# Optimization experiments

Measured on AMD Instinct MI355X. Metric: run time of the kernel, lower is better.

Reference implementation:

```python
import jax, jax.numpy as jnp
import numpy as np

# ---- config (matches init_kwargs) ----
C_IN, C_OUT = 128, 128
HYPER_OUT = 64            # hyper_out_size in DoubleConv
KB = C_IN // HYPER_OUT    # k = 2 blocks along input channels
HB = C_OUT // HYPER_OUT   # h = 2 blocks along output channels
Z_DIM, HID, SEIDEL_DIM = 128, 128, 48
R, F = 8, 3               # num_radii, filter size
BN_EPS = 1e-5


def _mlp_bank(z, W1, b1, W2, b2):
    # z: (S,); W1: (M,S,HID); returns (M, HID) embeddings from M distinct MLPs
    h = jax.nn.relu(jnp.einsum('s,msh->mh', z, W1) + b1)
    return jax.nn.relu(jnp.einsum('mh,mhg->mg', h, W2) + b2)


def _hyper(e, hw2, hb2, hw1, hb1):
    # Ha-style hypernetwork: e (Z_DIM,) -> kernel (64, 64, R, F, F)
    h_in = (e @ hw2 + hb2).reshape(HYPER_OUT, Z_DIM)
    h_fin = h_in @ hw1 + hb1  # (64, 64*R*F*F)
    return h_fin.reshape(HYPER_OUT, HYPER_OUT, R, F, F)


def _assemble(kernels, rows, cols):
    # kernels: (rows*cols, 64, 64, R, F, F) -> (rows*64, cols*64, R, F, F)
    k = kernels.reshape(rows, cols, HYPER_OUT, HYPER_OUT, R, F, F)
    k = k.transpose(0, 2, 1, 3, 4, 5, 6)
    return k.reshape(rows * HYPER_OUT, cols * HYPER_OUT, R, F, F)


def _interp_radii(w, Wdim):
    # trilinear interpolate (R,F,F)->(Wdim,F,F); F->F is identity, so linear along R
    # align_corners=False (PyTorch default)
    src = (jnp.arange(Wdim, dtype=jnp.float32) + 0.5) * (R / Wdim) - 0.5
    src = jnp.clip(src, 0.0, R - 1.0)
    i0 = jnp.floor(src).astype(jnp.int32)
    i1 = jnp.minimum(i0 + 1, R - 1)
    t = (src - i0.astype(jnp.float32))[None, None, :, None, None]
    return w[:, :, i0] * (1.0 - t) + w[:, :, i1] * t  # (co, ci, Wdim, F, F)


def _lri_conv(x, w):
    # x: (c_in, H, W); w: (c_out, c_in, R, F, F); padding=1, k=3
    c_in, H, W = x.shape
    xp = jnp.concatenate([x[:, -1:, :], x, x[:, :1, :]], axis=1)  # circular pad H
    xp = jnp.pad(xp, ((0, 0), (0, 0), (1, 1)))                    # zero pad W
    # patches laid out (c, di, dj) to match F.unfold
    pat = jnp.stack([xp[:, di:di + H, dj:dj + W]
                     for di in range(3) for dj in range(3)], axis=1)  # (c_in, 9, H, W)
    pat = pat.reshape(c_in * 9, H, W).transpose(1, 2, 0)              # (H, W, c_in*9)
    wi = _interp_radii(w, W)                                          # (co, ci, W, F, F)
    wu = wi.transpose(0, 2, 1, 3, 4).reshape(w.shape[0], W, c_in * 9) # (co, W, ci*9)
    return jnp.einsum('hwj,cwj->chw', pat, wu)                        # (co, H, W)


def _bn_eval(x, gamma, beta):
    # eval-mode BatchNorm2d with running_mean=0, running_var=1
    scale = gamma / jnp.sqrt(1.0 + BN_EPS)
    return x * scale[:, None, None] + beta[:, None, None]


def setup_inputs() -> dict:
    key = jax.random.key(0)
    ks = jax.random.split(key, 20)
    B, H, W = 2, 256, 128
    n1 = HB * KB   # 4 MLPs for first conv
    n2 = HB * HB   # 4 MLPs for second conv
    inp = {
        'x': jax.random.normal(ks[0], (B, C_IN, H, W), jnp.float32),
        'seidel': jax.random.normal(ks[1], (B, SEIDEL_DIM), jnp.float32),
        'm1_W1': jax.random.normal(ks[2], (n1, SEIDEL_DIM, HID)) * 0.1,
        'm1_b1': jnp.zeros((n1, HID)),
        'm1_W2': jax.random.normal(ks[3], (n1, HID, HID)) * 0.08,
        'm1_b2': jnp.zeros((n1, HID)),
        'm2_W1': jax.random.normal(ks[4], (n2, SEIDEL_DIM, HID)) * 0.1,
        'm2_b1': jnp.zeros((n2, HID)),
        'm2_W2': jax.random.normal(ks[5], (n2, HID, HID)) * 0.08,
        'm2_b2': jnp.zeros((n2, HID)),
        'hyp_w2': jax.random.normal(ks[6], (Z_DIM, HYPER_OUT * Z_DIM)) * 0.02,
        'hyp_b2': jnp.zeros((HYPER_OUT * Z_DIM,)),
        'hyp_w1': jax.random.normal(ks[7], (Z_DIM, HYPER_OUT * R * F * F)) * 0.02,
        'hyp_b1': jnp.zeros((HYPER_OUT * R * F * F,)),
        'bn1_g': jnp.ones((C_OUT,)), 'bn1_b': jnp.zeros((C_OUT,)),
        'bn2_g': jnp.ones((C_OUT,)), 'bn2_b': jnp.zeros((C_OUT,)),
    }
    return inp


def reference(x, seidel, m1_W1, m1_b1, m1_W2, m1_b2, m2_W1, m2_b1, m2_W2, m2_b2,
              hyp_w2, hyp_b2, hyp_w1, hyp_b1, bn1_g, bn1_b, bn2_g, bn2_b):
    hyper = lambda e: _hyper(e, hyp_w2, hyp_b2, hyp_w1, hyp_b1)

    def one_sample(x_i, z_i):
        emb1 = _mlp_bank(z_i, m1_W1, m1_b1, m1_W2, m1_b2)   # (h*k, Z)
        w1 = _assemble(jax.vmap(hyper)(emb1), HB, KB)        # (c_out, c_in, R, F, F)
        emb2 = _mlp_bank(z_i, m2_W1, m2_b1, m2_W2, m2_b2)   # (h*h, Z)
        w2 = _assemble(jax.vmap(hyper)(emb2), HB, HB)        # (c_out, c_out, R, F, F)
        y = jax.nn.relu(_bn_eval(_lri_conv(x_i, w1), bn1_g, bn1_b))
        y = jax.nn.relu(_bn_eval(_lri_conv(y, w2), bn2_g, bn2_b))
        return y

    return jax.vmap(one_sample)(x, seidel)  # (B, c_out, H, W)
```

## Files before the change

### kernel.cpp

```cpp
#include <hip/hip_runtime.h>
#include <hip/hip_bf16.h>

typedef _Float16 f16;
typedef _Float16 half8 __attribute__((ext_vector_type(8)));
typedef _Float16 half4_t __attribute__((ext_vector_type(4)));
typedef float floatx16 __attribute__((ext_vector_type(16)));

__global__ __launch_bounds__(256) void embed_a(
    const float* __restrict__ seidel,
    const float* __restrict__ m1W1, const float* __restrict__ m1b1,
    const float* __restrict__ m1W2, const float* __restrict__ m1b2,
    const float* __restrict__ m2W1, const float* __restrict__ m2b1,
    const float* __restrict__ m2W2, const float* __restrict__ m2b2,
    float* __restrict__ eout)
{
    int combo = blockIdx.x;
    int s = combo >> 3, conv = (combo >> 2) & 1, m = combo & 3;
    const float* W1 = conv ? m2W1 : m1W1;
    const float* b1 = conv ? m2b1 : m1b1;
    const float* W2 = conv ? m2W2 : m1W2;
    const float* b2 = conv ? m2b2 : m1b2;
    __shared__ float zs[48], hbuf[128];
    int tid = threadIdx.x;
    if (tid < 48) zs[tid] = seidel[s*48 + tid];
    __syncthreads();
    if (tid < 128) {
        float a = b1[m*128 + tid];
        for (int i = 0; i < 48; ++i) a += zs[i] * W1[(m*48 + i)*128 + tid];
        hbuf[tid] = fmaxf(a, 0.f);
    }
    __syncthreads();
    if (tid < 128) {
        float a = b2[m*128 + tid];
        for (int i = 0; i < 128; ++i) a += hbuf[i] * W2[(m*128 + i)*128 + tid];
        eout[combo*128 + tid] = fmaxf(a, 0.f);
    }
}

__global__ __launch_bounds__(256) void embed_b(
    const float* __restrict__ eout, const float* __restrict__ hw2,
    const float* __restrict__ hb2, float* __restrict__ hin)
{
    int combo = blockIdx.y;
    int j = blockIdx.x*256 + threadIdx.x;
    __shared__ float es[128];
    if (threadIdx.x < 128) es[threadIdx.x] = eout[combo*128 + threadIdx.x];
    __syncthreads();
    float a = hb2[j];
    for (int i = 0; i < 128; ++i) a += es[i] * hw2[(size_t)i*8192 + j];
    hin[(size_t)combo*8192 + j] = a;
}

__global__ void hw1t_kernel(const float* __restrict__ in, float* __restrict__ out)
{
    __shared__ float tile[32][33];
    int j0 = blockIdx.x*32, k0 = blockIdx.y*32;
    int tx = threadIdx.x, ty = threadIdx.y;
    #pragma unroll
    for (int i = 0; i < 4; ++i) tile[ty + i*8][tx] = in[(size_t)(k0 + ty + i*8)*4608 + j0 + tx];
    __syncthreads();
    #pragma unroll
    for (int i = 0; i < 4; ++i) out[(size_t)(j0 + ty + i*8)*128 + k0 + tx] = tile[tx][ty + i*8];
}

__global__ __launch_bounds__(256) void hfin2_kernel(
    const float* __restrict__ hin, const float* __restrict__ hw1t,
    const float* __restrict__ hb1, f16* __restrict__ wtab)
{
    int c72 = blockIdx.x;
    int combo = blockIdx.y;
    int r = c72 / 9, tap = c72 - r*9;
    int s = combo >> 3, conv = (combo >> 2) & 1, m = combo & 3;
    __shared__ float hl[64][132];
    __shared__ float wt[64][132];
    __shared__ f16 ct[64][72];
    int tid = threadIdx.x;
    const float4* hsrc = (const float4*)(hin + (size_t)combo*8192);
    for (int i = tid; i < 2048; i += 256) {
        int a = i >> 5, kq = i & 31;
        *(float4*)&hl[a][kq*4] = hsrc[i];
    }
    for (int i = tid; i < 2048; i += 256) {
        int b = i >> 5, kq = i & 31;
        *(float4*)&wt[b][kq*4] = *(const float4*)(hw1t + (size_t)(b*72 + c72)*128 + kq*4);
    }
    __syncthreads();
    int ta = tid >> 4, tb = tid & 15;
    int a0 = ta*4, b0 = tb*4;
    float acc[4][4] = {};
    #pragma unroll 4
    for (int k4 = 0; k4 < 32; ++k4) {
        float4 A[4], B[4];
        #pragma unroll
        for (int i = 0; i < 4; ++i) A[i] = *(const float4*)&hl[a0 + i][k4*4];
        #pragma unroll
        for (int i = 0; i < 4; ++i) B[i] = *(const float4*)&wt[b0 + i][k4*4];
        #pragma unroll
        for (int i = 0; i < 4; ++i)
            #pragma unroll
            for (int j2 = 0; j2 < 4; ++j2)
                acc[i][j2] += A[i].x*B[j2].x + A[i].y*B[j2].y + A[i].z*B[j2].z + A[i].w*B[j2].w;
    }
    float bj[4];
    #pragma unroll
    for (int j2 = 0; j2 < 4; ++j2) bj[j2] = hb1[(b0 + j2)*72 + c72];
    #pragma unroll
    for (int i = 0; i < 4; ++i) {
        half4_t v;
        #pragma unroll
        for (int j2 = 0; j2 < 4; ++j2) v[j2] = (f16)(acc[i][j2] + bj[j2]);
        *(half4_t*)&ct[a0 + i][b0] = v;
    }
    __syncthreads();
    {
        int run = tid >> 1, hh = tid & 1;
        int a = run & 63, ch = run >> 6;
        int chunk = (m & 1)*2 + ch;
        int co = (m >> 1)*64 + a;
        size_t base = ((((size_t)(s*2 + conv)*8 + r)*4 + chunk)*9 + tap)*128 + co;
        f16* dst = wtab + base*32 + hh*16;
        const f16* src = &ct[a][ch*32 + hh*16];
        *(half8*)(dst)     = *(const half8*)(src);
        *(half8*)(dst + 8) = *(const half8*)(src + 8);
    }
}

__global__ __launch_bounds__(256) void xpose_cast2(
    const float* __restrict__ in, f16* __restrict__ out)
{
    __shared__ f16 tileT[128*136];
    int h = blockIdx.x, s = blockIdx.y;
    int tid = threadIdx.x;
    int cg = tid >> 5, q2 = tid & 31;
    const float* src = in + (size_t)s*4194304 + (size_t)h*128;
    for (int pass = 0; pass < 16; ++pass) {
        int c = pass*8 + cg;
        float4 v = *(const float4*)(src + (size_t)c*32768 + q2*4);
        tileT[(q2*4 + 0)*136 + c] = (f16)v.x;
        tileT[(q2*4 + 1)*136 + c] = (f16)v.y;
        tileT[(q2*4 + 2)*136 + c] = (f16)v.z;
        tileT[(q2*4 + 3)*136 + c] = (f16)v.w;
    }
    __syncthreads();
    int ww = tid >> 1, hf = tid & 1;
    const f16* srcT = &tileT[ww*136 + hf*64];
    f16* dst = out + (((size_t)(s*128 + ww)*256 + h)*128) + hf*64;
    #pragma unroll
    for (int i = 0; i < 8; ++i)
        *(float4*)(dst + i*8) = *(const float4*)(srcT + i*8);
}

__global__ void xpose_out(const float* __restrict__ in, float* __restrict__ out)
{
    __shared__ float tile[32][33];
    int sc = blockIdx.z;
    int w0 = blockIdx.x*32, h0 = blockIdx.y*32;
    int tx = threadIdx.x, ty = threadIdx.y;
    const float* src = in + ((size_t)sc*128 + w0)*256 + h0;
    #pragma unroll
    for (int i = 0; i < 4; ++i) tile[ty + i*8][tx] = src[(size_t)(ty + i*8)*256 + tx];
    __syncthreads();
    float* dst = out + ((size_t)sc*256 + h0)*128 + w0;
    #pragma unroll
    for (int i = 0; i < 4; ++i) dst[(size_t)(ty + i*8)*128 + tx] = tile[tx][ty + i*8];
}

template<int OUT_F16>
__global__ __launch_bounds__(512, 2) void conv_mfma4(
    const f16* __restrict__ xin,
    const f16* __restrict__ wtab,
    int conv,
    const float* __restrict__ bng, const float* __restrict__ bnb,
    void* __restrict__ outp)
{
    int bx = blockIdx.x, s = blockIdx.y;
    int w = ((bx & 7) << 4) | (bx >> 3);
    const f16* xs  = xin  + (size_t)s*4194304;
    const f16* wts = wtab + (size_t)(s*2 + conv)*1179648;

    float fsrc = (w + 0.5f)*0.0625f - 0.5f;
    fsrc = fminf(fmaxf(fsrc, 0.f), 7.f);
    int r0 = (int)fsrc;
    int r1 = min(r0 + 1, 7);
    float t = fsrc - (float)r0;
    f16 th = (f16)t;

    __shared__ __align__(16) char sbuf[123264];
    f16* smW = (f16*)sbuf;
    f16* smX = (f16*)(sbuf + 73728);

    int tid = threadIdx.x;
    int lane = tid & 63, wid = tid >> 6;
    int wc = wid & 1, wh = wid >> 1;
    int l31 = lane & 31, lq = lane >> 5;

    floatx16 acc[2][2];
    #pragma unroll
    for (int a = 0; a < 2; ++a)
        #pragma unroll
        for (int b = 0; b < 2; ++b) acc[a][b] = (floatx16)0.f;

    int spart = tid >> 7, sco = tid & 127;

    for (int chunk = 0; chunk < 4; ++chunk) {
        __syncthreads();
        #pragma unroll
        for (int it = 0; it < 7; ++it) {
            int id = tid + it*512;
            if (id < 3096) {
                int dj = id / 1032;
                int r2 = id - dj*1032;
                int part = r2 & 3, hp = r2 >> 2;
                int wsg = w + dj - 1;
                half8 v = {};
                if (wsg >= 0 && wsg < 128) {
                    int hsrc = (hp - 1) & 255;
                    v = *(const half8*)(xs + ((size_t)wsg*256 + hsrc)*128 + chunk*32 + part*8);
                }
                *(half8*)(smX + (size_t)((dj*4 + part)*258 + hp)*8) = v;
            }
        }
        #pragma unroll
        for (int tap = 0; tap < 9; ++tap) {
            size_t o0 = (((size_t)(r0*4 + chunk)*9 + tap)*128 + sco)*32 + spart*8;
            size_t o1 = (((size_t)(r1*4 + chunk)*9 + tap)*128 + sco)*32 + spart*8;
            half8 a = *(const half8*)(wts + o0);
            half8 b = *(const half8*)(wts + o1);
            half8 o = a + (b - a)*th;
            *(half8*)(smW + (size_t)((tap*4 + spart)*128 + sco)*8) = o;
        }
        __syncthreads();
        #pragma unroll
        for (int tap = 0; tap < 9; ++tap) {
            int di = tap/3, dj = tap - di*3;
            half8 af[2][2], bf[2][2];
            #pragma unroll
            for (int ks = 0; ks < 2; ++ks) {
                #pragma unroll
                for (int ct = 0; ct < 2; ++ct)
                    af[ks][ct] = *(const half8*)(smW +
                        (size_t)((tap*4 + ks*2 + lq)*128 + wc*64 + ct*32 + l31)*8);
                #pragma unroll
                for (int ht = 0; ht < 2; ++ht)
                    bf[ks][ht] = *(const half8*)(smX +
                        (size_t)((dj*4 + ks*2 + lq)*258 + wh*64 + ht*32 + l31 + di)*8);
            }
            #pragma unroll
            for (int ks = 0; ks < 2; ++ks)
                #pragma unroll
                for (int ct = 0; ct < 2; ++ct)
                    #pragma unroll
                    for (int ht = 0; ht < 2; ++ht)
                        acc[ct][ht] = __builtin_amdgcn_mfma_f32_32x32x16_f16(
                            af[ks][ct], bf[ks][ht], acc[ct][ht], 0, 0, 0);
        }
    }

    float rs = rsqrtf(1.f + 1e-5f);
    if (OUT_F16) {
        f16* otile = (f16*)sbuf;
        f16* yout = (f16*)outp + ((size_t)(s*128 + w)*256)*128;
        #pragma unroll
        for (int ph = 0; ph < 2; ++ph) {
            __syncthreads();
            if ((wh >> 1) == ph) {
                #pragma unroll
                for (int ct = 0; ct < 2; ++ct) {
                    #pragma unroll
                    for (int ht = 0; ht < 2; ++ht) {
                        int hrow = (wh & 1)*64 + ht*32 + l31;
                        #pragma unroll
                        for (int rq = 0; rq < 4; ++rq) {
                            int cb = wc*64 + ct*32 + rq*8 + lq*4;
                            float4 g4 = *(const float4*)&bng[cb];
                            float4 b4 = *(const float4*)&bnb[cb];
                            half4_t v;
                            #pragma unroll
                            for (int e = 0; e < 4; ++e) {
                                float g = (&g4.x)[e], bb = (&b4.x)[e];
                                v[e] = (f16)fmaxf(acc[ct][ht][rq*4 + e]*g*rs + bb, 0.f);
                            }
                            *(half4_t*)&otile[hrow*136 + cb] = v;
                        }
                    }
                }
            }
            __syncthreads();
            {
                int hrow = tid >> 2, qc = tid & 3;
                const f16* srcT = &otile[hrow*136 + qc*32];
                f16* d = yout + (size_t)(ph*128 + hrow)*128 + qc*32;
                #pragma unroll
                for (int i = 0; i < 4; ++i)
                    *(float4*)(d + i*8) = *(const float4*)(srcT + i*8);
            }
        }
    } else {
        #pragma unroll
        for (int ct = 0; ct < 2; ++ct) {
            #pragma unroll
            for (int ht = 0; ht < 2; ++ht) {
                int hrow = wh*64 + ht*32 + l31;
                #pragma unroll
                for (int r = 0; r < 16; ++r) {
                    int co = wc*64 + ct*32 + (r & 3) + 8*(r >> 2) + 4*lq;
                    float v = fmaxf(acc[ct][ht][r]*bng[co]*rs + bnb[co], 0.f);
                    ((float*)outp)[((size_t)(s*128 + co)*128 + w)*256 + hrow] = v;
                }
            }
        }
    }
}

extern "C" void kernel_launch(void* const* d_in, const int* in_sizes, int n_in,
                              void* d_out, int out_size, void* d_ws, size_t ws_size,
                              hipStream_t stream) {
    const float* x      = (const float*)d_in[0];
    const float* seidel = (const float*)d_in[1];
    const float* m1W1 = (const float*)d_in[2];
    const float* m1b1 = (const float*)d_in[3];
    const float* m1W2 = (const float*)d_in[4];
    const float* m1b2 = (const float*)d_in[5];
    const float* m2W1 = (const float*)d_in[6];
    const float* m2b1 = (const float*)d_in[7];
    const float* m2W2 = (const float*)d_in[8];
    const float* m2b2 = (const float*)d_in[9];
    const float* hw2  = (const float*)d_in[10];
    const float* hb2  = (const float*)d_in[11];
    const float* hw1  = (const float*)d_in[12];
    const float* hb1  = (const float*)d_in[13];
    const float* bn1g = (const float*)d_in[14];
    const float* bn1b = (const float*)d_in[15];
    const float* bn2g = (const float*)d_in[16];
    const float* bn2b = (const float*)d_in[17];
    float* outp = (float*)d_out;

    char* wsb = (char*)d_ws;
    float* hin  = (float*)wsb;
    f16*   wtab = (f16*)(wsb + 524288);
    f16*   xt   = (f16*)(wsb + 9961472);
    f16*   y1t  = (f16*)(wsb + 26738688);
    float* y2t  = (float*)(wsb + 43515904);
    float* eout = (float*)xt;
    float* hw1t = y2t;

    embed_a<<<16, 256, 0, stream>>>(seidel, m1W1, m1b1, m1W2, m1b2,
                                    m2W1, m2b1, m2W2, m2b2, eout);
    embed_b<<<dim3(32, 16), 256, 0, stream>>>(eout, hw2, hb2, hin);
    hw1t_kernel<<<dim3(144, 4), dim3(32, 8), 0, stream>>>(hw1, hw1t);
    hfin2_kernel<<<dim3(72, 16), 256, 0, stream>>>(hin, hw1t, hb1, wtab);
    xpose_cast2<<<dim3(256, 2), 256, 0, stream>>>(x, xt);
    conv_mfma4<1><<<dim3(128, 2), 512, 0, stream>>>(xt, wtab, 0, bn1g, bn1b, (void*)y1t);
    conv_mfma4<0><<<dim3(128, 2), 512, 0, stream>>>(y1t, wtab, 1, bn2g, bn2b, (void*)y2t);
    xpose_out<<<dim3(4, 8, 256), dim3(32, 8), 0, stream>>>(y2t, outp);
}
```

Measured before the change: 156.5 us.

## Split conv blocks along H, shrink channel chunks, batch embed_b over combos

The conv kernel now uses 256-thread blocks that each cover half the H rows, and loops over 8 input-channel chunks of 16 instead of 4 of 32. This cuts shared memory per block enough to allow more resident blocks and gives twice as many blocks for the 256 CUs. The weight table layout in hfin2 changes to 16-channel chunks to match, and s_setprio is raised around the MFMA loop. embed_b now computes all 16 combos per thread so each hw2 element is read once, at the cost of fewer blocks. Weight interpolation and global reads are repeated per H-half and per chunk, which adds redundant traffic and more barriers.

```diff
diff --git a/kernel.cpp b/kernel.cpp
--- a/kernel.cpp
+++ b/kernel.cpp
@@ -37,18 +37,26 @@
     }
 }
 
-__global__ __launch_bounds__(256) void embed_b(
+__global__ __launch_bounds__(256) void embed_b2(
     const float* __restrict__ eout, const float* __restrict__ hw2,
     const float* __restrict__ hb2, float* __restrict__ hin)
 {
-    int combo = blockIdx.y;
-    int j = blockIdx.x*256 + threadIdx.x;
-    __shared__ float es[128];
-    if (threadIdx.x < 128) es[threadIdx.x] = eout[combo*128 + threadIdx.x];
-    __syncthreads();
-    float a = hb2[j];
-    for (int i = 0; i < 128; ++i) a += es[i] * hw2[(size_t)i*8192 + j];
-    hin[(size_t)combo*8192 + j] = a;
+    __shared__ float es[16][128];
+    int tid = threadIdx.x;
+    int j = blockIdx.x*256 + tid;
+    for (int i = tid; i < 2048; i += 256) es[i >> 7][i & 127] = eout[i];
+    __syncthreads();
+    float acc[16];
+    float b = hb2[j];
+    #pragma unroll
+    for (int c = 0; c < 16; ++c) acc[c] = b;
+    for (int i = 0; i < 128; ++i) {
+        float wv = hw2[(size_t)i*8192 + j];
+        #pragma unroll
+        for (int c = 0; c < 16; ++c) acc[c] += es[c][i]*wv;
+    }
+    #pragma unroll
+    for (int c = 0; c < 16; ++c) hin[(size_t)c*8192 + j] = acc[c];
 }
 
 __global__ void hw1t_kernel(const float* __restrict__ in, float* __restrict__ out)
@@ -113,15 +121,13 @@
     }
     __syncthreads();
     {
-        int run = tid >> 1, hh = tid & 1;
-        int a = run & 63, ch = run >> 6;
-        int chunk = (m & 1)*2 + ch;
+        int a = tid >> 2, q = tid & 3;
+        int hc = (m & 1)*4 + q;
         int co = (m >> 1)*64 + a;
-        size_t base = ((((size_t)(s*2 + conv)*8 + r)*4 + chunk)*9 + tap)*128 + co;
-        f16* dst = wtab + base*32 + hh*16;
-        const f16* src = &ct[a][ch*32 + hh*16];
-        *(half8*)(dst)     = *(const half8*)(src);
-        *(half8*)(dst + 8) = *(const half8*)(src + 8);
+        size_t base = ((((size_t)(s*2 + conv)*8 + r)*8 + hc)*9 + tap)*128 + co;
+        f16* dst = wtab + base*16;
+        *(half8*)(dst)     = *(const half8*)&ct[a][q*16];
+        *(half8*)(dst + 8) = *(const half8*)&ct[a][q*16 + 8];
     }
 }
 
@@ -166,33 +172,33 @@
 }
 
 template<int OUT_F16>
-__global__ __launch_bounds__(512, 2) void conv_mfma4(
+__global__ __launch_bounds__(256, 3) void conv_mfma5(
     const f16* __restrict__ xin,
     const f16* __restrict__ wtab,
     int conv,
     const float* __restrict__ bng, const float* __restrict__ bnb,
     void* __restrict__ outp)
 {
-    int bx = blockIdx.x, s = blockIdx.y;
+    int bx = blockIdx.x, hh = blockIdx.y, s = blockIdx.z;
     int w = ((bx & 7) << 4) | (bx >> 3);
+    int hbase = hh << 7;
     const f16* xs  = xin  + (size_t)s*4194304;
     const f16* wts = wtab + (size_t)(s*2 + conv)*1179648;
 
-    float fsrc = (w + 0.5f)*0.0625f - 0.5f;
-    fsrc = fminf(fmaxf(fsrc, 0.f), 7.f);
+    float fsrc = fminf(fmaxf((w + 0.5f)*0.0625f - 0.5f, 0.f), 7.f);
     int r0 = (int)fsrc;
     int r1 = min(r0 + 1, 7);
-    float t = fsrc - (float)r0;
-    f16 th = (f16)t;
-
-    __shared__ __align__(16) char sbuf[123264];
+    f16 th = (f16)(fsrc - (float)r0);
+
+    __shared__ __align__(16) char sbuf[49344];
     f16* smW = (f16*)sbuf;
-    f16* smX = (f16*)(sbuf + 73728);
+    f16* smX = (f16*)(sbuf + 36864);
 
     int tid = threadIdx.x;
     int lane = tid & 63, wid = tid >> 6;
     int wc = wid & 1, wh = wid >> 1;
     int l31 = lane & 31, lq = lane >> 5;
+    int spart = tid >> 7, sco = tid & 127;
 
     floatx16 acc[2][2];
     #pragma unroll
@@ -200,100 +206,79 @@
         #pragma unroll
         for (int b = 0; b < 2; ++b) acc[a][b] = (floatx16)0.f;
 
-    int spart = tid >> 7, sco = tid & 127;
-
-    for (int chunk = 0; chunk < 4; ++chunk) {
+    for (int hc = 0; hc < 8; ++hc) {
+        int ci0 = hc*16;
         __syncthreads();
-        #pragma unroll
-        for (int it = 0; it < 7; ++it) {
-            int id = tid + it*512;
-            if (id < 3096) {
-                int dj = id / 1032;
-                int r2 = id - dj*1032;
-                int part = r2 & 3, hp = r2 >> 2;
-                int wsg = w + dj - 1;
-                half8 v = {};
-                if (wsg >= 0 && wsg < 128) {
-                    int hsrc = (hp - 1) & 255;
-                    v = *(const half8*)(xs + ((size_t)wsg*256 + hsrc)*128 + chunk*32 + part*8);
-                }
-                *(half8*)(smX + (size_t)((dj*4 + part)*258 + hp)*8) = v;
+        for (int id = tid; id < 780; id += 256) {
+            int strip = id / 130;
+            int hp = id - strip*130;
+            int dj = strip >> 1, part = strip & 1;
+            int wsg = w + dj - 1;
+            half8 v = {};
+            if (wsg >= 0 && wsg < 128) {
+                int hsrc = (hbase + hp - 1) & 255;
+                v = *(const half8*)(xs + ((size_t)wsg*256 + hsrc)*128 + ci0 + part*8);
             }
+            *(half8*)(smX + (size_t)id*8) = v;
         }
         #pragma unroll
         for (int tap = 0; tap < 9; ++tap) {
-            size_t o0 = (((size_t)(r0*4 + chunk)*9 + tap)*128 + sco)*32 + spart*8;
-            size_t o1 = (((size_t)(r1*4 + chunk)*9 + tap)*128 + sco)*32 + spart*8;
-            half8 a = *(const half8*)(wts + o0);
-            half8 b = *(const half8*)(wts + o1);
+            const f16* p0 = wts + ((((size_t)r0*8 + hc)*9 + tap)*128 + sco)*16 + spart*8;
+            const f16* p1 = wts + ((((size_t)r1*8 + hc)*9 + tap)*128 + sco)*16 + spart*8;
+            half8 a = *(const half8*)p0;
+            half8 b = *(const half8*)p1;
             half8 o = a + (b - a)*th;
-            *(half8*)(smW + (size_t)((tap*4 + spart)*128 + sco)*8) = o;
+            *(half8*)(smW + (size_t)((tap*2 + spart)*128 + sco)*8) = o;
         }
         __syncthreads();
+        __builtin_amdgcn_s_setprio(1);
         #pragma unroll
         for (int tap = 0; tap < 9; ++tap) {
             int di = tap/3, dj = tap - di*3;
-            half8 af[2][2], bf[2][2];
-            #pragma unroll
-            for (int ks = 0; ks < 2; ++ks) {
-                #pragma unroll
-                for (int ct = 0; ct < 2; ++ct)
-                    af[ks][ct] = *(const half8*)(smW +
-                        (size_t)((tap*4 + ks*2 + lq)*128 + wc*64 + ct*32 + l31)*8);
-                #pragma unroll
-                for (int ht = 0; ht < 2; ++ht)
-                    bf[ks][ht] = *(const half8*)(smX +
-                        (size_t)((dj*4 + ks*2 + lq)*258 + wh*64 + ht*32 + l31 + di)*8);
-            }
-            #pragma unroll
-            for (int ks = 0; ks < 2; ++ks)
-                #pragma unroll
-                for (int ct = 0; ct < 2; ++ct)
-                    #pragma unroll
-                    for (int ht = 0; ht < 2; ++ht)
-                        acc[ct][ht] = __builtin_amdgcn_mfma_f32_32x32x16_f16(
-                            af[ks][ct], bf[ks][ht], acc[ct][ht], 0, 0, 0);
-        }
+            half8 af0 = *(const half8*)(smW + (size_t)((tap*2 + lq)*128 + wc*64 + l31)*8);
+            half8 af1 = *(const half8*)(smW + (size_t)((tap*2 + lq)*128 + wc*64 + 32 + l31)*8);
+            half8 bf0 = *(const half8*)(smX + (size_t)((dj*2 + lq)*130 + wh*64 + l31 + di)*8);
+            half8 bf1 = *(const half8*)(smX + (size_t)((dj*2 + lq)*130 + wh*64 + 32 + l31 + di)*8);
+            acc[0][0] = __builtin_amdgcn_mfma_f32_32x32x16_f16(af0, bf0, acc[0][0], 0, 0, 0);
+            acc[0][1] = __builtin_amdgcn_mfma_f32_32x32x16_f16(af0, bf1, acc[0][1], 0, 0, 0);
+            acc[1][0] = __builtin_amdgcn_mfma_f32_32x32x16_f16(af1, bf0, acc[1][0], 0, 0, 0);
+            acc[1][1] = __builtin_amdgcn_mfma_f32_32x32x16_f16(af1, bf1, acc[1][1], 0, 0, 0);
+        }
+        __builtin_amdgcn_s_setprio(0);
     }
 
     float rs = rsqrtf(1.f + 1e-5f);
     if (OUT_F16) {
+        __syncthreads();
         f16* otile = (f16*)sbuf;
-        f16* yout = (f16*)outp + ((size_t)(s*128 + w)*256)*128;
-        #pragma unroll
-        for (int ph = 0; ph < 2; ++ph) {
-            __syncthreads();
-            if ((wh >> 1) == ph) {
+        #pragma unroll
+        for (int ct = 0; ct < 2; ++ct) {
+            #pragma unroll
+            for (int ht = 0; ht < 2; ++ht) {
+                int hrow = wh*64 + ht*32 + l31;
                 #pragma unroll
-                for (int ct = 0; ct < 2; ++ct) {
+                for (int rq = 0; rq < 4; ++rq) {
+                    int cb = wc*64 + ct*32 + rq*8 + lq*4;
+                    float4 g4 = *(const float4*)&bng[cb];
+                    float4 b4 = *(const float4*)&bnb[cb];
+                    half4_t v;
                     #pragma unroll
-                    for (int ht = 0; ht < 2; ++ht) {
-                        int hrow = (wh & 1)*64 + ht*32 + l31;
-                        #pragma unroll
-                        for (int rq = 0; rq < 4; ++rq) {
-                            int cb = wc*64 + ct*32 + rq*8 + lq*4;
-                            float4 g4 = *(const float4*)&bng[cb];
-                            float4 b4 = *(const float4*)&bnb[cb];
-                            half4_t v;
-                            #pragma unroll
-                            for (int e = 0; e < 4; ++e) {
-                                float g = (&g4.x)[e], bb = (&b4.x)[e];
-                                v[e] = (f16)fmaxf(acc[ct][ht][rq*4 + e]*g*rs + bb, 0.f);
-                            }
-                            *(half4_t*)&otile[hrow*136 + cb] = v;
-                        }
+                    for (int e = 0; e < 4; ++e) {
+                        float g = (&g4.x)[e], bb = (&b4.x)[e];
+                        v[e] = (f16)fmaxf(acc[ct][ht][rq*4 + e]*g*rs + bb, 0.f);
                     }
+                    *(half4_t*)&otile[hrow*136 + cb] = v;
                 }
             }
-            __syncthreads();
-            {
-                int hrow = tid >> 2, qc = tid & 3;
-                const f16* srcT = &otile[hrow*136 + qc*32];
-                f16* d = yout + (size_t)(ph*128 + hrow)*128 + qc*32;
-                #pragma unroll
-                for (int i = 0; i < 4; ++i)
-                    *(float4*)(d + i*8) = *(const float4*)(srcT + i*8);
-            }
+        }
+        __syncthreads();
+        {
+            int hrow = tid >> 1, hf = tid & 1;
+            const f16* srcT = &otile[hrow*136 + hf*64];
+            f16* d = (f16*)outp + (((size_t)(s*128 + w)*256 + hbase + hrow))*128 + hf*64;
+            #pragma unroll
+            for (int i = 0; i < 8; ++i)
+                *(float4*)(d + i*8) = *(const float4*)(srcT + i*8);
         }
     } else {
         #pragma unroll
@@ -305,7 +290,7 @@
                 for (int r = 0; r < 16; ++r) {
                     int co = wc*64 + ct*32 + (r & 3) + 8*(r >> 2) + 4*lq;
                     float v = fmaxf(acc[ct][ht][r]*bng[co]*rs + bnb[co], 0.f);
-                    ((float*)outp)[((size_t)(s*128 + co)*128 + w)*256 + hrow] = v;
+                    ((float*)outp)[((size_t)(s*128 + co)*128 + w)*256 + hbase + hrow] = v;
                 }
             }
         }
@@ -346,11 +331,11 @@
 
     embed_a<<<16, 256, 0, stream>>>(seidel, m1W1, m1b1, m1W2, m1b2,
                                     m2W1, m2b1, m2W2, m2b2, eout);
-    embed_b<<<dim3(32, 16), 256, 0, stream>>>(eout, hw2, hb2, hin);
+    embed_b2<<<32, 256, 0, stream>>>(eout, hw2, hb2, hin);
     hw1t_kernel<<<dim3(144, 4), dim3(32, 8), 0, stream>>>(hw1, hw1t);
     hfin2_kernel<<<dim3(72, 16), 256, 0, stream>>>(hin, hw1t, hb1, wtab);
     xpose_cast2<<<dim3(256, 2), 256, 0, stream>>>(x, xt);
-    conv_mfma4<1><<<dim3(128, 2), 512, 0, stream>>>(xt, wtab, 0, bn1g, bn1b, (void*)y1t);
-    conv_mfma4<0><<<dim3(128, 2), 512, 0, stream>>>(y1t, wtab, 1, bn2g, bn2b, (void*)y2t);
+    conv_mfma5<1><<<dim3(128, 2, 2), 256, 0, stream>>>(xt, wtab, 0, bn1g, bn1b, (void*)y1t);
+    conv_mfma5<0><<<dim3(128, 2, 2), 256, 0, stream>>>(y1t, wtab, 1, bn2g, bn2b, (void*)y2t);
     xpose_out<<<dim3(4, 8, 256), dim3(32, 8), 0, stream>>>(y2t, outp);
 }
```

New measurement: 163.9 us. +4.8%, slower.

## Double-buffer conv input tiles and read interpolated weights directly from global

Applied to the files above, without the earlier changes.

The conv kernel now prefetches the next channel chunk of the input into registers while MFMAs run on the current chunk, then stores it into a second LDS buffer. This replaces two barriers per chunk with one and hides global load latency. Weights are no longer staged in LDS: each wave loads both radius slices from global and interpolates in registers, which raises global/L2 traffic but frees LDS. Separately, embed_b is restructured so each block computes all 16 combos and reads each hw2 element once instead of sixteen times.

```diff
diff --git a/kernel.cpp b/kernel.cpp
--- a/kernel.cpp
+++ b/kernel.cpp
@@ -37,18 +37,26 @@
     }
 }
 
-__global__ __launch_bounds__(256) void embed_b(
+__global__ __launch_bounds__(256) void embed_b2(
     const float* __restrict__ eout, const float* __restrict__ hw2,
     const float* __restrict__ hb2, float* __restrict__ hin)
 {
-    int combo = blockIdx.y;
-    int j = blockIdx.x*256 + threadIdx.x;
-    __shared__ float es[128];
-    if (threadIdx.x < 128) es[threadIdx.x] = eout[combo*128 + threadIdx.x];
-    __syncthreads();
-    float a = hb2[j];
-    for (int i = 0; i < 128; ++i) a += es[i] * hw2[(size_t)i*8192 + j];
-    hin[(size_t)combo*8192 + j] = a;
+    __shared__ float es[16][128];
+    int tid = threadIdx.x;
+    int j = blockIdx.x*256 + tid;
+    for (int i = tid; i < 2048; i += 256) es[i >> 7][i & 127] = eout[i];
+    __syncthreads();
+    float acc[16];
+    float b = hb2[j];
+    #pragma unroll
+    for (int c = 0; c < 16; ++c) acc[c] = b;
+    for (int i = 0; i < 128; ++i) {
+        float wv = hw2[(size_t)i*8192 + j];
+        #pragma unroll
+        for (int c = 0; c < 16; ++c) acc[c] += es[c][i]*wv;
+    }
+    #pragma unroll
+    for (int c = 0; c < 16; ++c) hin[(size_t)c*8192 + j] = acc[c];
 }
 
 __global__ void hw1t_kernel(const float* __restrict__ in, float* __restrict__ out)
@@ -166,7 +174,7 @@
 }
 
 template<int OUT_F16>
-__global__ __launch_bounds__(512, 2) void conv_mfma4(
+__global__ __launch_bounds__(512, 2) void conv_mfma6(
     const f16* __restrict__ xin,
     const f16* __restrict__ wtab,
     int conv,
@@ -178,16 +186,13 @@
     const f16* xs  = xin  + (size_t)s*4194304;
     const f16* wts = wtab + (size_t)(s*2 + conv)*1179648;
 
-    float fsrc = (w + 0.5f)*0.0625f - 0.5f;
-    fsrc = fminf(fmaxf(fsrc, 0.f), 7.f);
+    float fsrc = fminf(fmaxf((w + 0.5f)*0.0625f - 0.5f, 0.f), 7.f);
     int r0 = (int)fsrc;
     int r1 = min(r0 + 1, 7);
-    float t = fsrc - (float)r0;
-    f16 th = (f16)t;
-
-    __shared__ __align__(16) char sbuf[123264];
-    f16* smW = (f16*)sbuf;
-    f16* smX = (f16*)(sbuf + 73728);
+    f16 th = (f16)(fsrc - (float)r0);
+
+    __shared__ __align__(16) char sbuf[99072];
+    f16* smX = (f16*)sbuf;
 
     int tid = threadIdx.x;
     int lane = tid & 63, wid = tid >> 6;
@@ -200,51 +205,71 @@
         #pragma unroll
         for (int b = 0; b < 2; ++b) acc[a][b] = (floatx16)0.f;
 
-    int spart = tid >> 7, sco = tid & 127;
+    half8 xr[7];
+    #pragma unroll
+    for (int it = 0; it < 7; ++it) {
+        int id = tid + it*512;
+        if (id < 3096) {
+            int dj = id / 1032, r2 = id - dj*1032;
+            int part = r2 & 3, hp = r2 >> 2;
+            int wsg = w + dj - 1;
+            half8 v = {};
+            if (wsg >= 0 && wsg < 128)
+                v = *(const half8*)(xs + ((size_t)wsg*256 + ((hp - 1) & 255))*128 + part*8);
+            xr[it] = v;
+        }
+    }
+    #pragma unroll
+    for (int it = 0; it < 7; ++it) {
+        int id = tid + it*512;
+        if (id < 3096) {
+            int dj = id / 1032, r2 = id - dj*1032;
+            int part = r2 & 3, hp = r2 >> 2;
+            *(half8*)(smX + (size_t)((dj*4 + part)*258 + hp)*8) = xr[it];
+        }
+    }
+    __syncthreads();
 
     for (int chunk = 0; chunk < 4; ++chunk) {
-        __syncthreads();
-        #pragma unroll
-        for (int it = 0; it < 7; ++it) {
-            int id = tid + it*512;
-            if (id < 3096) {
-                int dj = id / 1032;
-                int r2 = id - dj*1032;
-                int part = r2 & 3, hp = r2 >> 2;
-                int wsg = w + dj - 1;
-                half8 v = {};
-                if (wsg >= 0 && wsg < 128) {
-                    int hsrc = (hp - 1) & 255;
-                    v = *(const half8*)(xs + ((size_t)wsg*256 + hsrc)*128 + chunk*32 + part*8);
-                }
-                *(half8*)(smX + (size_t)((dj*4 + part)*258 + hp)*8) = v;
-            }
-        }
-        #pragma unroll
-        for (int tap = 0; tap < 9; ++tap) {
-            size_t o0 = (((size_t)(r0*4 + chunk)*9 + tap)*128 + sco)*32 + spart*8;
-            size_t o1 = (((size_t)(r1*4 + chunk)*9 + tap)*128 + sco)*32 + spart*8;
-            half8 a = *(const half8*)(wts + o0);
-            half8 b = *(const half8*)(wts + o1);
-            half8 o = a + (b - a)*th;
-            *(half8*)(smW + (size_t)((tap*4 + spart)*128 + sco)*8) = o;
-        }
-        __syncthreads();
+        const f16* bufX = smX + (chunk & 1)*24768;
+        if (chunk < 3) {
+            #pragma unroll
+            for (int it = 0; it < 7; ++it) {
+                int id = tid + it*512;
+                if (id < 3096) {
+                    int dj = id / 1032, r2 = id - dj*1032;
+                    int part = r2 & 3, hp = r2 >> 2;
+                    int wsg = w + dj - 1;
+                    half8 v = {};
+                    if (wsg >= 0 && wsg < 128)
+                        v = *(const half8*)(xs + ((size_t)wsg*256 + ((hp - 1) & 255))*128
+                                            + (chunk + 1)*32 + part*8);
+                    xr[it] = v;
+                }
+            }
+        }
         #pragma unroll
         for (int tap = 0; tap < 9; ++tap) {
             int di = tap/3, dj = tap - di*3;
-            half8 af[2][2], bf[2][2];
-            #pragma unroll
-            for (int ks = 0; ks < 2; ++ks) {
-                #pragma unroll
-                for (int ct = 0; ct < 2; ++ct)
-                    af[ks][ct] = *(const half8*)(smW +
-                        (size_t)((tap*4 + ks*2 + lq)*128 + wc*64 + ct*32 + l31)*8);
+            const f16* w0p = wts + ((((size_t)r0*4 + chunk)*9 + tap) << 12);
+            const f16* w1p = wts + ((((size_t)r1*4 + chunk)*9 + tap) << 12);
+            half8 af[2][2];
+            #pragma unroll
+            for (int ks = 0; ks < 2; ++ks)
+                #pragma unroll
+                for (int ct = 0; ct < 2; ++ct) {
+                    int co = wc*64 + ct*32 + l31;
+                    half8 a = *(const half8*)(w0p + co*32 + ks*16 + lq*8);
+                    half8 b = *(const half8*)(w1p + co*32 + ks*16 + lq*8);
+                    af[ks][ct] = a + (b - a)*th;
+                }
+            half8 bf[2][2];
+            #pragma unroll
+            for (int ks = 0; ks < 2; ++ks)
                 #pragma unroll
                 for (int ht = 0; ht < 2; ++ht)
-                    bf[ks][ht] = *(const half8*)(smX +
+                    bf[ks][ht] = *(const half8*)(bufX +
                         (size_t)((dj*4 + ks*2 + lq)*258 + wh*64 + ht*32 + l31 + di)*8);
-            }
             #pragma unroll
             for (int ks = 0; ks < 2; ++ks)
                 #pragma unroll
@@ -254,6 +279,19 @@
                         acc[ct][ht] = __builtin_amdgcn_mfma_f32_32x32x16_f16(
                             af[ks][ct], bf[ks][ht], acc[ct][ht], 0, 0, 0);
         }
+        if (chunk < 3) {
+            f16* dstX = smX + ((chunk + 1) & 1)*24768;
+            #pragma unroll
+            for (int it = 0; it < 7; ++it) {
+                int id = tid + it*512;
+                if (id < 3096) {
+                    int dj = id / 1032, r2 = id - dj*1032;
+                    int part = r2 & 3, hp = r2 >> 2;
+                    *(half8*)(dstX + (size_t)((dj*4 + part)*258 + hp)*8) = xr[it];
+                }
+            }
+        }
+        __syncthreads();
     }
 
     float rs = rsqrtf(1.f + 1e-5f);
@@ -346,11 +384,11 @@
 
     embed_a<<<16, 256, 0, stream>>>(seidel, m1W1, m1b1, m1W2, m1b2,
                                     m2W1, m2b1, m2W2, m2b2, eout);
-    embed_b<<<dim3(32, 16), 256, 0, stream>>>(eout, hw2, hb2, hin);
+    embed_b2<<<32, 256, 0, stream>>>(eout, hw2, hb2, hin);
     hw1t_kernel<<<dim3(144, 4), dim3(32, 8), 0, stream>>>(hw1, hw1t);
     hfin2_kernel<<<dim3(72, 16), 256, 0, stream>>>(hin, hw1t, hb1, wtab);
     xpose_cast2<<<dim3(256, 2), 256, 0, stream>>>(x, xt);
-    conv_mfma4<1><<<dim3(128, 2), 512, 0, stream>>>(xt, wtab, 0, bn1g, bn1b, (void*)y1t);
-    conv_mfma4<0><<<dim3(128, 2), 512, 0, stream>>>(y1t, wtab, 1, bn2g, bn2b, (void*)y2t);
+    conv_mfma6<1><<<dim3(128, 2), 512, 0, stream>>>(xt, wtab, 0, bn1g, bn1b, (void*)y1t);
+    conv_mfma6<0><<<dim3(128, 2), 512, 0, stream>>>(y1t, wtab, 1, bn2g, bn2b, (void*)y2t);
     xpose_out<<<dim3(4, 8, 256), dim3(32, 8), 0, stream>>>(y2t, outp);
 }
```

After: 186.4 us. +19.1%, slower.
